# Kernel tuning notes

Measured on AMD Instinct MI355X. Metric: run time of the kernel, lower is better.

## Reference

```python
import jax, jax.numpy as jnp
import numpy as np

M, N, D, B, LAYERS = 512, 512, 1024, 4096, 16


def setup_inputs() -> dict:
    key = jax.random.key(0)
    ks = jax.random.split(key, 4)
    x = jax.random.normal(ks[0], (M, B), dtype=jnp.float32)
    A = jax.random.normal(ks[1], (M, D), dtype=jnp.float32) / np.float32(np.sqrt(M))
    # fc[k].weight = A.t() + 0.001*randn  -> shape [d, m]
    W = A.T[None] + 0.001 * jax.random.normal(ks[2], (LAYERS, D, M), dtype=jnp.float32)
    Z0 = (1.0 / D) * jax.random.uniform(ks[3], (D, B), dtype=jnp.float32)
    E0 = jnp.zeros((M, B), dtype=jnp.float32)
    L0 = jnp.zeros((M, B), dtype=jnp.float32)
    ones = jnp.ones((LAYERS,), dtype=jnp.float32)
    return {
        'x': x, 'A': A, 'W': W, 'Z0': Z0, 'E0': E0, 'L0': L0,
        'beta1': ones, 'beta2': ones, 'beta3': ones, 'ss2': ones,
        'active_para': 0.2 * ones, 'active_para1': 0.8 * ones,
    }


def _soft(v, t):
    # self_active: relu(v - t) - relu(-v - t)  (soft threshold)
    return jax.nn.relu(v - t) - jax.nn.relu(-v - t)


def reference(x, A, W, Z0, E0, L0, beta1, beta2, beta3, ss2, active_para, active_para1):
    K = W.shape[0]
    # k = 0 (learned branch)
    T0 = A @ Z0 + E0 - x                      # [m, B]
    Var0 = L0 + beta1[0] * T0
    Z1 = _soft(Z0 - W[0] @ Var0, active_para[0])  # [d, B]

    def step(carry, params):
        Zp, Ep, Lp = carry
        b1, b2, b3, s2, ap, ap1, Wk = params
        AZ = A @ Zp                            # [m, B]
        VVar = Lp + b2 * (AZ + Ep - x)
        En = _soft(Ep - s2 * VVar, ap1)
        Tn = AZ + En - x
        Ln = Lp + b3 * Tn
        Varn = Ln + b1 * Tn
        Zn = _soft(Zp - Wk @ Varn, ap)
        return (Zn, En, Ln), (Zn, En, Ln)

    params = (beta1[1:], beta2[:K - 1], beta3[:K - 1], ss2[:K - 1],
              active_para[1:], active_para1[:K - 1], W[1:])
    _, (Zs, Es, Ls) = jax.lax.scan(step, (Z1, E0, L0), params)
    Z_all = jnp.concatenate([Z1[None], Zs], axis=0)   # [K, d, B]
    E_all = jnp.concatenate([E0[None], Es], axis=0)   # [K, m, B]
    L_all = jnp.concatenate([L0[None], Ls], axis=0)   # [K, m, B]
    return Z_all, E_all, L_all
```

## Files before the change

### kernel.cpp

```cpp
#include <hip/hip_runtime.h>
#include <cstddef>

#define MDIM 512
#define DDIM 1024
#define BDIM 4096
#define NLAYERS 16

constexpr int BM = 64, BN = 128, BK = 16, TM = 4, TN = 8;
constexpr int NTH = (BM / TM) * (BN / TN);

__device__ __forceinline__ float softf(float v, float t) {
  return copysignf(fmaxf(fabsf(v) - t, 0.0f), v);
}

template <int MODE>
__global__ __launch_bounds__(NTH) void fused_gemm(
    const float* __restrict__ P, const float* __restrict__ Q, int K,
    const float* __restrict__ x, const float* __restrict__ Ep,
    const float* __restrict__ Lp, const float* __restrict__ Zp,
    const float* __restrict__ beta1, const float* __restrict__ beta2,
    const float* __restrict__ beta3, const float* __restrict__ ss2,
    const float* __restrict__ apar, const float* __restrict__ apar1, int k,
    float* __restrict__ O0, float* __restrict__ O1, float* __restrict__ O2) {
  __shared__ __align__(16) float As[BK][BM];
  __shared__ __align__(16) float Bs[BK][BN];

  const int tid = threadIdx.x;
  const int m0 = blockIdx.x * BM;
  const int n0 = blockIdx.y * BN;
  const int tn = tid & 15, tm = tid >> 4;

  const int arow = tid >> 2;
  const int acol = (tid & 3) * 4;
  const int brow = tid >> 4;
  const int bcol = (tid & 15) * 8;

  float acc[TM][TN];
#pragma unroll
  for (int i = 0; i < TM; ++i)
#pragma unroll
    for (int j = 0; j < TN; ++j) acc[i][j] = 0.0f;

  const float* pA = &P[(size_t)(m0 + arow) * K + acol];
  const float* pB = &Q[(size_t)brow * BDIM + n0 + bcol];

  for (int k0 = 0; k0 < K; k0 += BK) {
    const float4 av = *reinterpret_cast<const float4*>(pA + k0);
    const float4 bv0 = *reinterpret_cast<const float4*>(pB + (size_t)k0 * BDIM);
    const float4 bv1 = *reinterpret_cast<const float4*>(pB + (size_t)k0 * BDIM + 4);
    __syncthreads();
    As[acol + 0][arow] = av.x;
    As[acol + 1][arow] = av.y;
    As[acol + 2][arow] = av.z;
    As[acol + 3][arow] = av.w;
    *reinterpret_cast<float4*>(&Bs[brow][bcol]) = bv0;
    *reinterpret_cast<float4*>(&Bs[brow][bcol + 4]) = bv1;
    __syncthreads();
#pragma unroll
    for (int kk = 0; kk < BK; ++kk) {
      const float4 a4 = *reinterpret_cast<const float4*>(&As[kk][tm * TM]);
      const float4 b4 = *reinterpret_cast<const float4*>(&Bs[kk][tn * TN]);
      const float4 b5 = *reinterpret_cast<const float4*>(&Bs[kk][tn * TN + 4]);
      const float a[TM] = {a4.x, a4.y, a4.z, a4.w};
      const float b[TN] = {b4.x, b4.y, b4.z, b4.w, b5.x, b5.y, b5.z, b5.w};
#pragma unroll
      for (int i = 0; i < TM; ++i)
#pragma unroll
        for (int j = 0; j < TN; ++j) acc[i][j] = fmaf(a[i], b[j], acc[i][j]);
    }
  }

  const int row0 = m0 + tm * TM;
  const int col0 = n0 + tn * TN;

  if (MODE == 2) {
    const float ap = apar[k];
#pragma unroll
    for (int i = 0; i < TM; ++i) {
      const size_t off = (size_t)(row0 + i) * BDIM + col0;
      const float4 z0 = *reinterpret_cast<const float4*>(&Zp[off]);
      const float4 z1 = *reinterpret_cast<const float4*>(&Zp[off + 4]);
      float4 o0, o1;
      o0.x = softf(z0.x - acc[i][0], ap);
      o0.y = softf(z0.y - acc[i][1], ap);
      o0.z = softf(z0.z - acc[i][2], ap);
      o0.w = softf(z0.w - acc[i][3], ap);
      o1.x = softf(z1.x - acc[i][4], ap);
      o1.y = softf(z1.y - acc[i][5], ap);
      o1.z = softf(z1.z - acc[i][6], ap);
      o1.w = softf(z1.w - acc[i][7], ap);
      *reinterpret_cast<float4*>(&O0[off]) = o0;
      *reinterpret_cast<float4*>(&O0[off + 4]) = o1;
    }
  } else {
    const float b1v = beta1[k];
    float b2v = 0.f, b3v = 0.f, s2v = 0.f, a1v = 0.f;
    if (MODE == 1) {
      b2v = beta2[k - 1];
      b3v = beta3[k - 1];
      s2v = ss2[k - 1];
      a1v = apar1[k - 1];
    }
#pragma unroll
    for (int i = 0; i < TM; ++i) {
      const size_t off = (size_t)(row0 + i) * BDIM + col0;
      float ev[TN], lv[TN], xv[TN];
      *reinterpret_cast<float4*>(&ev[0]) = *reinterpret_cast<const float4*>(&Ep[off]);
      *reinterpret_cast<float4*>(&ev[4]) = *reinterpret_cast<const float4*>(&Ep[off + 4]);
      *reinterpret_cast<float4*>(&lv[0]) = *reinterpret_cast<const float4*>(&Lp[off]);
      *reinterpret_cast<float4*>(&lv[4]) = *reinterpret_cast<const float4*>(&Lp[off + 4]);
      *reinterpret_cast<float4*>(&xv[0]) = *reinterpret_cast<const float4*>(&x[off]);
      *reinterpret_cast<float4*>(&xv[4]) = *reinterpret_cast<const float4*>(&x[off + 4]);
      float vo[TN], eo[TN], lo_[TN];
#pragma unroll
      for (int j = 0; j < TN; ++j) {
        const float az = acc[i][j];
        if (MODE == 0) {
          const float t0 = az + ev[j] - xv[j];
          vo[j] = fmaf(b1v, t0, lv[j]);
          eo[j] = ev[j];
          lo_[j] = lv[j];
        } else {
          const float vv = fmaf(b2v, az + ev[j] - xv[j], lv[j]);
          const float en = softf(ev[j] - s2v * vv, a1v);
          const float tn_ = az + en - xv[j];
          const float ln = fmaf(b3v, tn_, lv[j]);
          eo[j] = en;
          lo_[j] = ln;
          vo[j] = fmaf(b1v, tn_, ln);
        }
      }
      *reinterpret_cast<float4*>(&O0[off]) = *reinterpret_cast<const float4*>(&vo[0]);
      *reinterpret_cast<float4*>(&O0[off + 4]) = *reinterpret_cast<const float4*>(&vo[4]);
      *reinterpret_cast<float4*>(&O1[off]) = *reinterpret_cast<const float4*>(&eo[0]);
      *reinterpret_cast<float4*>(&O1[off + 4]) = *reinterpret_cast<const float4*>(&eo[4]);
      *reinterpret_cast<float4*>(&O2[off]) = *reinterpret_cast<const float4*>(&lo_[0]);
      *reinterpret_cast<float4*>(&O2[off + 4]) = *reinterpret_cast<const float4*>(&lo_[4]);
    }
  }
}

extern "C" void kernel_launch(void* const* d_in, const int* in_sizes, int n_in,
                              void* d_out, int out_size, void* d_ws,
                              size_t ws_size, hipStream_t stream) {
  (void)in_sizes;
  (void)n_in;
  (void)out_size;
  (void)ws_size;
  const float* x = (const float*)d_in[0];
  const float* A = (const float*)d_in[1];
  const float* W = (const float*)d_in[2];
  const float* Z0 = (const float*)d_in[3];
  const float* E0 = (const float*)d_in[4];
  const float* L0 = (const float*)d_in[5];
  const float* beta1 = (const float*)d_in[6];
  const float* beta2 = (const float*)d_in[7];
  const float* beta3 = (const float*)d_in[8];
  const float* ss2 = (const float*)d_in[9];
  const float* apar = (const float*)d_in[10];
  const float* apar1 = (const float*)d_in[11];

  constexpr size_t DB = (size_t)DDIM * BDIM;
  constexpr size_t MB = (size_t)MDIM * BDIM;
  float* Zall = (float*)d_out;
  float* Eall = Zall + (size_t)NLAYERS * DB;
  float* Lall = Eall + (size_t)NLAYERS * MB;
  float* Var = (float*)d_ws;

  const dim3 blk(NTH);
  const dim3 g1(MDIM / BM, BDIM / BN);
  const dim3 g2(DDIM / BM, BDIM / BN);

  fused_gemm<0><<<g1, blk, 0, stream>>>(A, Z0, DDIM, x, E0, L0, nullptr, beta1,
                                        beta2, beta3, ss2, apar, apar1, 0, Var,
                                        Eall, Lall);
  fused_gemm<2><<<g2, blk, 0, stream>>>(W, Var, MDIM, x, nullptr, nullptr, Z0,
                                        beta1, beta2, beta3, ss2, apar, apar1,
                                        0, Zall, nullptr, nullptr);
  for (int k = 1; k < NLAYERS; ++k) {
    const float* Zp = Zall + (size_t)(k - 1) * DB;
    fused_gemm<1><<<g1, blk, 0, stream>>>(
        A, Zp, DDIM, x, Eall + (size_t)(k - 1) * MB,
        Lall + (size_t)(k - 1) * MB, nullptr, beta1, beta2, beta3, ss2, apar,
        apar1, k, Var, Eall + (size_t)k * MB, Lall + (size_t)k * MB);
    fused_gemm<2><<<g2, blk, 0, stream>>>(
        W + (size_t)k * DDIM * MDIM, Var, MDIM, x, nullptr, nullptr, Zp, beta1,
        beta2, beta3, ss2, apar, apar1, k, Zall + (size_t)k * DB, nullptr,
        nullptr);
  }
}
```

Baseline: 2.440 ms.

## Double-buffer shared tiles and specialize GEMM tile width per stage

Rewrites the fused GEMM kernel with double-buffered LDS tiles so the next K-slice's global loads overlap the current slice's FMAs, using one barrier per iteration instead of two. K becomes a compile-time template parameter. The A*Z stage uses narrower 64-column tiles to get more blocks, while the W*Var stage keeps 128 columns. Thread-to-column mapping becomes strided 4-wide groups for conflict-free LDS reads, and the A tile is padded to 68 columns. The cost is twice the shared memory and more register pressure.

```diff
diff --git a/kernel.cpp b/kernel.cpp
--- a/kernel.cpp
+++ b/kernel.cpp
@@ -6,136 +6,149 @@
 #define BDIM 4096
 #define NLAYERS 16
 
-constexpr int BM = 64, BN = 128, BK = 16, TM = 4, TN = 8;
-constexpr int NTH = (BM / TM) * (BN / TN);
+constexpr int BK = 16;
 
 __device__ __forceinline__ float softf(float v, float t) {
   return copysignf(fmaxf(fabsf(v) - t, 0.0f), v);
 }
 
-template <int MODE>
-__global__ __launch_bounds__(NTH) void fused_gemm(
-    const float* __restrict__ P, const float* __restrict__ Q, int K,
-    const float* __restrict__ x, const float* __restrict__ Ep,
+template <int MODE, int K, int BN>
+__global__ __launch_bounds__(256) void gemm_f32(
+    const float* __restrict__ P, const float* __restrict__ Bm,
+    const float* __restrict__ xg, const float* __restrict__ Ep,
     const float* __restrict__ Lp, const float* __restrict__ Zp,
     const float* __restrict__ beta1, const float* __restrict__ beta2,
     const float* __restrict__ beta3, const float* __restrict__ ss2,
     const float* __restrict__ apar, const float* __restrict__ apar1, int k,
     float* __restrict__ O0, float* __restrict__ O1, float* __restrict__ O2) {
-  __shared__ __align__(16) float As[BK][BM];
-  __shared__ __align__(16) float Bs[BK][BN];
+  constexpr int TN = BN / 16;
+  constexpr int NG = BN / 64;
+  __shared__ __align__(16) float As[2][BK][68];
+  __shared__ __align__(16) float Bs[2][BK][BN];
 
   const int tid = threadIdx.x;
-  const int m0 = blockIdx.x * BM;
-  const int n0 = blockIdx.y * BN;
   const int tn = tid & 15, tm = tid >> 4;
-
-  const int arow = tid >> 2;
-  const int acol = (tid & 3) * 4;
-  const int brow = tid >> 4;
-  const int bcol = (tid & 15) * 8;
-
-  float acc[TM][TN];
-#pragma unroll
-  for (int i = 0; i < TM; ++i)
-#pragma unroll
-    for (int j = 0; j < TN; ++j) acc[i][j] = 0.0f;
-
-  const float* pA = &P[(size_t)(m0 + arow) * K + acol];
-  const float* pB = &Q[(size_t)brow * BDIM + n0 + bcol];
-
-  for (int k0 = 0; k0 < K; k0 += BK) {
-    const float4 av = *reinterpret_cast<const float4*>(pA + k0);
-    const float4 bv0 = *reinterpret_cast<const float4*>(pB + (size_t)k0 * BDIM);
-    const float4 bv1 = *reinterpret_cast<const float4*>(pB + (size_t)k0 * BDIM + 4);
+  const int m0 = blockIdx.x * 64, n0 = blockIdx.y * BN;
+
+  float acc[4][TN];
+#pragma unroll
+  for (int r = 0; r < 4; ++r)
+#pragma unroll
+    for (int c = 0; c < TN; ++c) acc[r][c] = 0.0f;
+
+  const int ar = tid >> 2, akc = tid & 3;
+  const float* gA = P + (size_t)(m0 + ar) * K + akc * 4;
+  const int br = (NG == 1) ? (tid >> 4) : (tid >> 5);
+  const int bc = (NG == 1) ? (tid & 15) : (tid & 31);
+  const float* gB = Bm + (size_t)br * BDIM + n0 + bc * 4;
+
+  float4 ra, rb0, rb1;
+  auto gload = [&](int k0) {
+    ra = *reinterpret_cast<const float4*>(gA + (size_t)k0);
+    rb0 = *reinterpret_cast<const float4*>(gB + (size_t)k0 * BDIM);
+    if (NG == 2)
+      rb1 = *reinterpret_cast<const float4*>(gB + (size_t)(k0 + 8) * BDIM);
+  };
+  auto stagewr = [&](int bb) {
+    As[bb][akc * 4 + 0][ar] = ra.x;
+    As[bb][akc * 4 + 1][ar] = ra.y;
+    As[bb][akc * 4 + 2][ar] = ra.z;
+    As[bb][akc * 4 + 3][ar] = ra.w;
+    *reinterpret_cast<float4*>(&Bs[bb][br][bc * 4]) = rb0;
+    if (NG == 2) *reinterpret_cast<float4*>(&Bs[bb][br + 8][bc * 4]) = rb1;
+  };
+  auto comp = [&](int bb) {
+#pragma unroll
+    for (int kk = 0; kk < BK; ++kk) {
+      const float4 a4 = *reinterpret_cast<const float4*>(&As[bb][kk][tm * 4]);
+      const float a[4] = {a4.x, a4.y, a4.z, a4.w};
+      float bv[TN];
+#pragma unroll
+      for (int g = 0; g < NG; ++g)
+        *reinterpret_cast<float4*>(&bv[g * 4]) =
+            *reinterpret_cast<const float4*>(&Bs[bb][kk][g * 64 + tn * 4]);
+#pragma unroll
+      for (int r = 0; r < 4; ++r)
+#pragma unroll
+        for (int c = 0; c < TN; ++c) acc[r][c] = fmaf(a[r], bv[c], acc[r][c]);
+    }
+  };
+
+  constexpr int NS = K / BK;
+  gload(0);
+  stagewr(0);
+  __syncthreads();
+  int bb = 0;
+#pragma unroll 1
+  for (int t = 1; t < NS; ++t) {
+    gload(t * BK);
+    comp(bb);
+    stagewr(bb ^ 1);
     __syncthreads();
-    As[acol + 0][arow] = av.x;
-    As[acol + 1][arow] = av.y;
-    As[acol + 2][arow] = av.z;
-    As[acol + 3][arow] = av.w;
-    *reinterpret_cast<float4*>(&Bs[brow][bcol]) = bv0;
-    *reinterpret_cast<float4*>(&Bs[brow][bcol + 4]) = bv1;
-    __syncthreads();
-#pragma unroll
-    for (int kk = 0; kk < BK; ++kk) {
-      const float4 a4 = *reinterpret_cast<const float4*>(&As[kk][tm * TM]);
-      const float4 b4 = *reinterpret_cast<const float4*>(&Bs[kk][tn * TN]);
-      const float4 b5 = *reinterpret_cast<const float4*>(&Bs[kk][tn * TN + 4]);
-      const float a[TM] = {a4.x, a4.y, a4.z, a4.w};
-      const float b[TN] = {b4.x, b4.y, b4.z, b4.w, b5.x, b5.y, b5.z, b5.w};
-#pragma unroll
-      for (int i = 0; i < TM; ++i)
-#pragma unroll
-        for (int j = 0; j < TN; ++j) acc[i][j] = fmaf(a[i], b[j], acc[i][j]);
-    }
-  }
-
-  const int row0 = m0 + tm * TM;
-  const int col0 = n0 + tn * TN;
-
-  if (MODE == 2) {
-    const float ap = apar[k];
-#pragma unroll
-    for (int i = 0; i < TM; ++i) {
-      const size_t off = (size_t)(row0 + i) * BDIM + col0;
-      const float4 z0 = *reinterpret_cast<const float4*>(&Zp[off]);
-      const float4 z1 = *reinterpret_cast<const float4*>(&Zp[off + 4]);
-      float4 o0, o1;
-      o0.x = softf(z0.x - acc[i][0], ap);
-      o0.y = softf(z0.y - acc[i][1], ap);
-      o0.z = softf(z0.z - acc[i][2], ap);
-      o0.w = softf(z0.w - acc[i][3], ap);
-      o1.x = softf(z1.x - acc[i][4], ap);
-      o1.y = softf(z1.y - acc[i][5], ap);
-      o1.z = softf(z1.z - acc[i][6], ap);
-      o1.w = softf(z1.w - acc[i][7], ap);
-      *reinterpret_cast<float4*>(&O0[off]) = o0;
-      *reinterpret_cast<float4*>(&O0[off + 4]) = o1;
-    }
-  } else {
-    const float b1v = beta1[k];
-    float b2v = 0.f, b3v = 0.f, s2v = 0.f, a1v = 0.f;
-    if (MODE == 1) {
-      b2v = beta2[k - 1];
-      b3v = beta3[k - 1];
-      s2v = ss2[k - 1];
-      a1v = apar1[k - 1];
-    }
-#pragma unroll
-    for (int i = 0; i < TM; ++i) {
-      const size_t off = (size_t)(row0 + i) * BDIM + col0;
-      float ev[TN], lv[TN], xv[TN];
-      *reinterpret_cast<float4*>(&ev[0]) = *reinterpret_cast<const float4*>(&Ep[off]);
-      *reinterpret_cast<float4*>(&ev[4]) = *reinterpret_cast<const float4*>(&Ep[off + 4]);
-      *reinterpret_cast<float4*>(&lv[0]) = *reinterpret_cast<const float4*>(&Lp[off]);
-      *reinterpret_cast<float4*>(&lv[4]) = *reinterpret_cast<const float4*>(&Lp[off + 4]);
-      *reinterpret_cast<float4*>(&xv[0]) = *reinterpret_cast<const float4*>(&x[off]);
-      *reinterpret_cast<float4*>(&xv[4]) = *reinterpret_cast<const float4*>(&x[off + 4]);
-      float vo[TN], eo[TN], lo_[TN];
-#pragma unroll
-      for (int j = 0; j < TN; ++j) {
-        const float az = acc[i][j];
-        if (MODE == 0) {
-          const float t0 = az + ev[j] - xv[j];
-          vo[j] = fmaf(b1v, t0, lv[j]);
-          eo[j] = ev[j];
-          lo_[j] = lv[j];
-        } else {
-          const float vv = fmaf(b2v, az + ev[j] - xv[j], lv[j]);
-          const float en = softf(ev[j] - s2v * vv, a1v);
-          const float tn_ = az + en - xv[j];
-          const float ln = fmaf(b3v, tn_, lv[j]);
-          eo[j] = en;
-          lo_[j] = ln;
-          vo[j] = fmaf(b1v, tn_, ln);
+    bb ^= 1;
+  }
+  comp(bb);
+
+  const float b1v = (MODE == 2) ? 0.f : beta1[k];
+  float b2v = 0.f, b3v = 0.f, s2v = 0.f, a1v = 0.f, ap = 0.f;
+  if (MODE == 1) {
+    b2v = beta2[k - 1];
+    b3v = beta3[k - 1];
+    s2v = ss2[k - 1];
+    a1v = apar1[k - 1];
+  }
+  if (MODE == 2) ap = apar[k];
+
+#pragma unroll
+  for (int r = 0; r < 4; ++r) {
+    const int row = m0 + tm * 4 + r;
+#pragma unroll
+    for (int g = 0; g < NG; ++g) {
+      const int col = n0 + g * 64 + tn * 4;
+      const size_t off = (size_t)row * BDIM + col;
+      if (MODE == 2) {
+        const float4 z4 = *reinterpret_cast<const float4*>(&Zp[off]);
+        const float z[4] = {z4.x, z4.y, z4.z, z4.w};
+        float4 o;
+        float* op = reinterpret_cast<float*>(&o);
+#pragma unroll
+        for (int j = 0; j < 4; ++j)
+          op[j] = softf(z[j] - acc[r][g * 4 + j], ap);
+        *reinterpret_cast<float4*>(&O0[off]) = o;
+      } else {
+        float ev[4], lv[4], xv[4];
+        *reinterpret_cast<float4*>(&ev[0]) =
+            *reinterpret_cast<const float4*>(&Ep[off]);
+        *reinterpret_cast<float4*>(&lv[0]) =
+            *reinterpret_cast<const float4*>(&Lp[off]);
+        *reinterpret_cast<float4*>(&xv[0]) =
+            *reinterpret_cast<const float4*>(&xg[off]);
+        float vo[4], eo[4], lo_[4];
+#pragma unroll
+        for (int j = 0; j < 4; ++j) {
+          const float az = acc[r][g * 4 + j];
+          if (MODE == 0) {
+            const float t0 = az + ev[j] - xv[j];
+            vo[j] = fmaf(b1v, t0, lv[j]);
+            eo[j] = ev[j];
+            lo_[j] = lv[j];
+          } else {
+            const float vv = fmaf(b2v, az + ev[j] - xv[j], lv[j]);
+            const float en = softf(ev[j] - s2v * vv, a1v);
+            const float tn_ = az + en - xv[j];
+            const float ln = fmaf(b3v, tn_, lv[j]);
+            eo[j] = en;
+            lo_[j] = ln;
+            vo[j] = fmaf(b1v, tn_, ln);
+          }
         }
+        *reinterpret_cast<float4*>(&O0[off]) =
+            *reinterpret_cast<const float4*>(&vo[0]);
+        *reinterpret_cast<float4*>(&O1[off]) =
+            *reinterpret_cast<const float4*>(&eo[0]);
+        *reinterpret_cast<float4*>(&O2[off]) =
+            *reinterpret_cast<const float4*>(&lo_[0]);
       }
-      *reinterpret_cast<float4*>(&O0[off]) = *reinterpret_cast<const float4*>(&vo[0]);
-      *reinterpret_cast<float4*>(&O0[off + 4]) = *reinterpret_cast<const float4*>(&vo[4]);
-      *reinterpret_cast<float4*>(&O1[off]) = *reinterpret_cast<const float4*>(&eo[0]);
-      *reinterpret_cast<float4*>(&O1[off + 4]) = *reinterpret_cast<const float4*>(&eo[4]);
-      *reinterpret_cast<float4*>(&O2[off]) = *reinterpret_cast<const float4*>(&lo_[0]);
-      *reinterpret_cast<float4*>(&O2[off + 4]) = *reinterpret_cast<const float4*>(&lo_[4]);
     }
   }
 }
@@ -167,24 +180,24 @@
   float* Lall = Eall + (size_t)NLAYERS * MB;
   float* Var = (float*)d_ws;
 
-  const dim3 blk(NTH);
-  const dim3 g1(MDIM / BM, BDIM / BN);
-  const dim3 g2(DDIM / BM, BDIM / BN);
-
-  fused_gemm<0><<<g1, blk, 0, stream>>>(A, Z0, DDIM, x, E0, L0, nullptr, beta1,
-                                        beta2, beta3, ss2, apar, apar1, 0, Var,
-                                        Eall, Lall);
-  fused_gemm<2><<<g2, blk, 0, stream>>>(W, Var, MDIM, x, nullptr, nullptr, Z0,
-                                        beta1, beta2, beta3, ss2, apar, apar1,
-                                        0, Zall, nullptr, nullptr);
+  const dim3 blk(256);
+  const dim3 gA(MDIM / 64, BDIM / 64);
+  const dim3 gB(DDIM / 64, BDIM / 128);
+
+  gemm_f32<0, DDIM, 64><<<gA, blk, 0, stream>>>(
+      A, Z0, x, E0, L0, nullptr, beta1, beta2, beta3, ss2, apar, apar1, 0, Var,
+      Eall, Lall);
+  gemm_f32<2, MDIM, 128><<<gB, blk, 0, stream>>>(
+      W, Var, nullptr, nullptr, nullptr, Z0, beta1, beta2, beta3, ss2, apar,
+      apar1, 0, Zall, nullptr, nullptr);
   for (int k = 1; k < NLAYERS; ++k) {
     const float* Zp = Zall + (size_t)(k - 1) * DB;
-    fused_gemm<1><<<g1, blk, 0, stream>>>(
-        A, Zp, DDIM, x, Eall + (size_t)(k - 1) * MB,
-        Lall + (size_t)(k - 1) * MB, nullptr, beta1, beta2, beta3, ss2, apar,
-        apar1, k, Var, Eall + (size_t)k * MB, Lall + (size_t)k * MB);
-    fused_gemm<2><<<g2, blk, 0, stream>>>(
-        W + (size_t)k * DDIM * MDIM, Var, MDIM, x, nullptr, nullptr, Zp, beta1,
+    gemm_f32<1, DDIM, 64><<<gA, blk, 0, stream>>>(
+        A, Zp, x, Eall + (size_t)(k - 1) * MB, Lall + (size_t)(k - 1) * MB,
+        nullptr, beta1, beta2, beta3, ss2, apar, apar1, k,
+        Var, Eall + (size_t)k * MB, Lall + (size_t)k * MB);
+    gemm_f32<2, MDIM, 128><<<gB, blk, 0, stream>>>(
+        W + (size_t)k * DDIM * MDIM, Var, nullptr, nullptr, nullptr, Zp, beta1,
         beta2, beta3, ss2, apar, apar1, k, Zall + (size_t)k * DB, nullptr,
         nullptr);
   }
```

Result: faster. 2.052 ms (-15.9%).
